# Kernel tuning notes

Hardware: AMD Instinct MI355X
Metric: run time of the kernel (lower is better)

The kernel has to match this reference:

```python
import jax, jax.numpy as jnp
import numpy as np

DT = 0.1
BOX = 1.0  # WORLD_SIZE
EPS = 1e-6


def range_angle(ang):
    return jnp.mod(ang + jnp.pi, 2.0 * jnp.pi) - jnp.pi


def ekf_step(x, P, a, Y, n1, n2_sigma, n2_kappa, gains, obs_gains):
    # x: (N,5) [px,py,ang,vel,ang_vel]; P: (N,5,5); a: (N,2); Y: (2,N)
    N = x.shape[0]
    dt = DT
    og = obs_gains

    # --- noise-free dynamics (w=0 in original forward) ---
    vel = gains[0] * a[:, 0]
    ang_vel = gains[1] * a[:, 1]
    ang = range_angle(x[:, 2] + ang_vel * dt)
    px = jnp.clip(x[:, 0] + vel * jnp.cos(ang) * dt, -BOX, BOX)
    py = jnp.clip(x[:, 1] + vel * jnp.sin(ang) * dt, -BOX, BOX)
    x_ = jnp.stack([px, py, ang, vel, ang_vel], axis=1)  # (N,5)

    # --- Jacobian A (N,5,5): eye(3) block + two trig entries ---
    d3 = jnp.arange(3)
    A = jnp.zeros((N, 5, 5), x.dtype)
    A = A.at[:, d3, d3].set(1.0)
    A = A.at[:, 0, 2].set(-vel * jnp.sin(ang) * dt)
    A = A.at[:, 1, 2].set(vel * jnp.cos(ang) * dt)

    # --- predict: L is identity in the original code, so L Q L^T = Q ---
    Q = jnp.diag(jnp.exp(2.0 * n1))
    P_ = jnp.einsum('nij,njk,nlk->nil', A, P, A) + Q  # (N,5,5)

    # --- innovation covariance S = H P_ H^T + M R M^T (R = I, M diag) ---
    # H = [0 | diag(og)] so H P_ H^T = diag(og) P_[3:5,3:5] diag(og)
    HPHt = P_[:, 3:5, 3:5] * og[None, :, None] * og[None, None, :]
    m_diag = x_[:, 3:5] ** 2 * jnp.exp(2.0 * n2_kappa) + jnp.exp(2.0 * n2_sigma)
    S = HPHt + m_diag[:, :, None] * jnp.eye(2, dtype=x.dtype)  # (N,2,2)

    # --- explicit 2x2 inverse ---
    sa, sb = S[:, 0, 0], S[:, 0, 1]
    sc, sd = S[:, 1, 0], S[:, 1, 1]
    det = sa * sd - sb * sc
    Sinv = jnp.stack([jnp.stack([sd, -sb], -1), jnp.stack([-sc, sa], -1)], -2)
    Sinv = Sinv / det[:, None, None]

    # --- Kalman gain K = P_ H^T S^{-1} ---
    PHt = P_[:, :, 3:5] * og[None, None, :]  # (N,5,2)
    K = jnp.einsum('nij,njk->nik', PHt, Sinv)  # (N,5,2)

    # --- update ---
    h = og[None, :] * x_[:, 3:5]  # noise-free observations (N,2)
    err = Y.T - h
    x_new = x_ + jnp.einsum('nij,nj->ni', K, err)

    KH = jnp.zeros((N, 5, 5), x.dtype).at[:, :, 3:5].set(K * og[None, None, :])
    I_KH = jnp.eye(5, dtype=x.dtype) - KH
    P_new = jnp.einsum('nij,njk->nik', I_KH, P_)
    P_new = 0.5 * (P_new + jnp.swapaxes(P_new, -1, -2)) + EPS * jnp.eye(5, dtype=x.dtype)
    return x_new, P_new, K


def setup_inputs() -> dict:
    key = jax.random.key(0)
    ks = jax.random.split(key, 6)
    N = 500_000
    x = jax.random.normal(ks[0], (N, 5), jnp.float32)
    # symmetric positive-definite covariances
    Lr = 0.1 * jax.random.normal(ks[1], (N, 5, 5), jnp.float32)
    P = jnp.einsum('nij,nkj->nik', Lr, Lr) + 0.5 * jnp.eye(5, dtype=jnp.float32)
    a = jax.random.normal(ks[2], (N, 2), jnp.float32)
    Y = 0.5 * jax.random.normal(ks[3], (2, N), jnp.float32)
    n1 = jnp.full((5,), -1.0, jnp.float32)
    n2 = jnp.full((4,), -1.0, jnp.float32)
    return {
        'x': x, 'P': P, 'a': a, 'Y': Y,
        'n1': n1,
        'n2_sigma': n2[:2],
        'n2_kappa': n2[2:],
        'gains': jnp.ones((2,), jnp.float32),
        'obs_gains': jnp.ones((2,), jnp.float32),
    }


def reference(x, P, a, Y, n1, n2_sigma, n2_kappa, gains, obs_gains):
    return ekf_step(x, P, a, Y, n1, n2_sigma, n2_kappa, gains, obs_gains)
```

## Files before the change

kernel.cpp:

```cpp
#include <hip/hip_runtime.h>
#include <math.h>
#include <stdint.h>


#define BLK 64
#define SLICE_F 2560

struct Pref {
    float4 p0, p1, p2, p3, p4, p5;
    float  pr;
    float4 x4;
    float  xr;
    float2 av;
    float  y0, y1;
};

__device__ __forceinline__ void load_pref(Pref& r,
    const float* __restrict__ Pg, const float* __restrict__ xg,
    const float* __restrict__ ag, const float* __restrict__ Yg,
    int N, int base, int l) {
    const float4* p4 = (const float4*)(Pg + (size_t)base * 25);
    r.p0 = p4[0 * 64 + l]; r.p1 = p4[1 * 64 + l]; r.p2 = p4[2 * 64 + l];
    r.p3 = p4[3 * 64 + l]; r.p4 = p4[4 * 64 + l]; r.p5 = p4[5 * 64 + l];
    r.pr = (Pg + (size_t)base * 25)[1536 + l];
    r.x4 = ((const float4*)(xg + (size_t)base * 5))[l];
    r.xr = (xg + (size_t)base * 5)[256 + l];
    r.av = ((const float2*)(ag + (size_t)base * 2))[l];
    r.y0 = Yg[base + l];
    r.y1 = Yg[N + base + l];
}

__device__ __forceinline__ void stage_write(const Pref& r, float* s, int l) {
    float4* s4 = (float4*)s;
    s4[0 * 64 + l] = r.p0; s4[1 * 64 + l] = r.p1; s4[2 * 64 + l] = r.p2;
    s4[3 * 64 + l] = r.p3; s4[4 * 64 + l] = r.p4; s4[5 * 64 + l] = r.p5;
    s[1536 + l] = r.pr;
    ((float4*)(s + 1600))[l] = r.x4;
    s[1856 + l] = r.xr;
}

struct EkfOut {
    float px, py, ang, xn3, xn4;
    float t00, s01, s02, t11, s12, t22, Pn33, Pn44;
    float K30, K41;
};

__device__ __forceinline__ EkfOut ekf_math(
    float x0, float x1, float x2, float a0, float a1, float y0, float y1,
    float p00, float p01, float p02, float p10, float p11, float p12,
    float p20, float p21, float p22,
    float g0, float g1, float og0, float og1,
    float q0, float q1, float q2, float q3, float q4,
    float e2s0, float e2s1, float e2k0, float e2k1)
{
    const float dt = 0.1f;
    const float fPI  = 3.14159265358979323846f;
    const float f2PI = 6.28318530717958647692f;
    const float EPS_ = 1e-6f;

    float vel = g0 * a0, angvel = g1 * a1;

    float ar = x2 + angvel * dt + fPI;
    float w = fmodf(ar, f2PI);
    if (w < 0.0f) w += f2PI;
    float ang = w - fPI;

    float s, c;
    sincosf(ang, &s, &c);

    EkfOut o;
    o.px = fminf(fmaxf(x0 + vel * c * dt, -1.0f), 1.0f);
    o.py = fminf(fmaxf(x1 + vel * s * dt, -1.0f), 1.0f);
    o.ang = ang;

    float m0 = -vel * s * dt, m1 = vel * c * dt;

    float b00 = p00 + m0 * p20, b01 = p01 + m0 * p21, b02 = p02 + m0 * p22;
    float b10 = p10 + m1 * p20, b11 = p11 + m1 * p21, b12 = p12 + m1 * p22;
    float t00 = b00 + m0 * b02, t01 = b01 + m1 * b02;
    float t10 = b10 + m0 * b12, t11 = b11 + m1 * b12;
    float t20 = p20 + m0 * p22, t21 = p21 + m1 * p22, t22 = p22;
    float t02 = b02, t12 = b12;

    t00 += q0; t11 += q1; t22 += q2;
    o.s01 = 0.5f * (t01 + t10);
    o.s02 = 0.5f * (t02 + t20);
    o.s12 = 0.5f * (t12 + t21);
    o.t00 = t00 + EPS_; o.t11 = t11 + EPS_; o.t22 = t22 + EPS_;

    float S00 = q3 * og0 * og0 + vel * vel * e2k0 + e2s0;
    float S11 = q4 * og1 * og1 + angvel * angvel * e2k1 + e2s1;
    o.K30 = q3 * og0 / S00;
    o.K41 = q4 * og1 / S11;

    o.xn3 = vel    + o.K30 * (y0 - og0 * vel);
    o.xn4 = angvel + o.K41 * (y1 - og1 * angvel);
    o.Pn33 = (1.0f - o.K30 * og0) * q3 + EPS_;
    o.Pn44 = (1.0f - o.K41 * og1) * q4 + EPS_;
    return o;
}

__global__ __launch_bounds__(256) void ekf_kernel(
    const float* __restrict__ xg, const float* __restrict__ Pg,
    const float* __restrict__ ag, const float* __restrict__ Yg,
    const float* __restrict__ n1, const float* __restrict__ n2s,
    const float* __restrict__ n2k, const float* __restrict__ gains,
    const float* __restrict__ og, float* __restrict__ out, int N)
{
    __shared__ float4 ldsv[4 * (SLICE_F / 4)];
    const int tid = threadIdx.x;
    const int wv = tid >> 6, l = tid & 63;
    float* s = (float*)ldsv + wv * SLICE_F;

    const int tiles = (N + BLK - 1) / BLK;
    const int NW = gridDim.x * 4;
    const int wp = blockIdx.x * 4 + wv;
    const int myTiles = (wp < tiles) ? (tiles - wp + NW - 1) / NW : 0;
    if (myTiles <= 0) return;

    const float g0 = gains[0], g1 = gains[1];
    const float og0 = og[0], og1 = og[1];
    const float q0 = expf(2.f * n1[0]), q1 = expf(2.f * n1[1]),
                q2 = expf(2.f * n1[2]), q3 = expf(2.f * n1[3]),
                q4 = expf(2.f * n1[4]);
    const float e2s0 = expf(2.f * n2s[0]), e2s1 = expf(2.f * n2s[1]);
    const float e2k0 = expf(2.f * n2k[0]), e2k1 = expf(2.f * n2k[1]);

    Pref A, B;
    {
        int b0 = wp * BLK;
        if (b0 + BLK <= N) load_pref(A, Pg, xg, ag, Yg, N, b0, l);
    }

    int k = 0;
    auto process = [&](Pref& cur, Pref& nxt) {
        const int base = (wp + k * NW) * BLK;
        if (base + BLK <= N) {
            stage_write(cur, s, l);
            if (k + 1 < myTiles) {
                int nb = (wp + (k + 1) * NW) * BLK;
                if (nb + BLK <= N) load_pref(nxt, Pg, xg, ag, Yg, N, nb, l);
            }
            const float* pr = s + l * 25;
            float p00 = pr[0], p01 = pr[1], p02 = pr[2];
            float p10 = pr[5], p11 = pr[6], p12 = pr[7];
            float p20 = pr[10], p21 = pr[11], p22 = pr[12];
            const float* xr = s + 1600 + l * 5;
            float x0 = xr[0], x1 = xr[1], x2 = xr[2];

            EkfOut o = ekf_math(x0, x1, x2, cur.av.x, cur.av.y, cur.y0, cur.y1,
                                p00, p01, p02, p10, p11, p12, p20, p21, p22,
                                g0, g1, og0, og1, q0, q1, q2, q3, q4,
                                e2s0, e2s1, e2k0, e2k1);

            float* xx = s + l * 5;
            xx[0] = o.px; xx[1] = o.py; xx[2] = o.ang; xx[3] = o.xn3; xx[4] = o.xn4;
            float* pp = s + 320 + l * 25;
            pp[0]  = o.t00; pp[1]  = o.s01; pp[2]  = o.s02; pp[3]  = 0.f; pp[4]  = 0.f;
            pp[5]  = o.s01; pp[6]  = o.t11; pp[7]  = o.s12; pp[8]  = 0.f; pp[9]  = 0.f;
            pp[10] = o.s02; pp[11] = o.s12; pp[12] = o.t22; pp[13] = 0.f; pp[14] = 0.f;
            pp[15] = 0.f;   pp[16] = 0.f;   pp[17] = 0.f;   pp[18] = o.Pn33; pp[19] = 0.f;
            pp[20] = 0.f;   pp[21] = 0.f;   pp[22] = 0.f;   pp[23] = 0.f;   pp[24] = o.Pn44;
            float* kk = s + 1920 + l * 10;
            kk[0] = 0.f; kk[1] = 0.f; kk[2] = 0.f; kk[3] = 0.f; kk[4] = 0.f;
            kk[5] = 0.f; kk[6] = o.K30; kk[7] = 0.f; kk[8] = 0.f; kk[9] = o.K41;

            float4* gx4 = (float4*)(out + (size_t)base * 5);
            float4* gp4 = (float4*)(out + (size_t)5 * N + (size_t)base * 25);
            float4* gk4 = (float4*)(out + (size_t)30 * N + (size_t)base * 10);
            const float4* lx4 = (const float4*)s;
            const float4* lp4 = (const float4*)(s + 320);
            const float4* lk4 = (const float4*)(s + 1920);
            gx4[l] = lx4[l];
            if (l < 16) gx4[64 + l] = lx4[64 + l];
            #pragma unroll
            for (int j = 0; j < 6; ++j) gp4[j * 64 + l] = lp4[j * 64 + l];
            if (l < 16) gp4[384 + l] = lp4[384 + l];
            #pragma unroll
            for (int j = 0; j < 2; ++j) gk4[j * 64 + l] = lk4[j * 64 + l];
            if (l < 32) gk4[128 + l] = lk4[128 + l];
        } else {
            const int i = base + l;
            if (i < N) {
                const float* pr = Pg + (size_t)i * 25;
                EkfOut o = ekf_math(xg[i * 5 + 0], xg[i * 5 + 1], xg[i * 5 + 2],
                                    ag[i * 2 + 0], ag[i * 2 + 1],
                                    Yg[i], Yg[N + i],
                                    pr[0], pr[1], pr[2], pr[5], pr[6], pr[7],
                                    pr[10], pr[11], pr[12],
                                    g0, g1, og0, og1, q0, q1, q2, q3, q4,
                                    e2s0, e2s1, e2k0, e2k1);
                float* gx = out + (size_t)i * 5;
                gx[0] = o.px; gx[1] = o.py; gx[2] = o.ang; gx[3] = o.xn3; gx[4] = o.xn4;
                float* gp = out + (size_t)5 * N + (size_t)i * 25;
                gp[0] = o.t00; gp[1] = o.s01; gp[2] = o.s02; gp[3] = 0.f; gp[4] = 0.f;
                gp[5] = o.s01; gp[6] = o.t11; gp[7] = o.s12; gp[8] = 0.f; gp[9] = 0.f;
                gp[10] = o.s02; gp[11] = o.s12; gp[12] = o.t22; gp[13] = 0.f; gp[14] = 0.f;
                gp[15] = 0.f; gp[16] = 0.f; gp[17] = 0.f; gp[18] = o.Pn33; gp[19] = 0.f;
                gp[20] = 0.f; gp[21] = 0.f; gp[22] = 0.f; gp[23] = 0.f; gp[24] = o.Pn44;
                float* gk = out + (size_t)30 * N + (size_t)i * 10;
                gk[0] = 0.f; gk[1] = 0.f; gk[2] = 0.f; gk[3] = 0.f; gk[4] = 0.f;
                gk[5] = 0.f; gk[6] = o.K30; gk[7] = 0.f; gk[8] = 0.f; gk[9] = o.K41;
            }
        }
    };

    while (true) {
        process(A, B);
        if (++k >= myTiles) break;
        process(B, A);
        if (++k >= myTiles) break;
    }
}

extern "C" void kernel_launch(void* const* d_in, const int* in_sizes, int n_in,
                              void* d_out, int out_size, void* d_ws, size_t ws_size,
                              hipStream_t stream) {
    const float* x     = (const float*)d_in[0];
    const float* P     = (const float*)d_in[1];
    const float* a     = (const float*)d_in[2];
    const float* Y     = (const float*)d_in[3];
    const float* n1    = (const float*)d_in[4];
    const float* n2s   = (const float*)d_in[5];
    const float* n2k   = (const float*)d_in[6];
    const float* gains = (const float*)d_in[7];
    const float* og    = (const float*)d_in[8];
    const int N = in_sizes[0] / 5;
    const int tiles = (N + BLK - 1) / BLK;
    int G = 768;
    if (G * 4 > tiles) G = (tiles + 3) / 4;
    ekf_kernel<<<G, 256, 0, stream>>>(x, P, a, Y, n1, n2s, n2k, gains, og,
                                      (float*)d_out, N);
}
```

Measured before the change: 171.8 us.

## Replace persistent grid-stride loop with one tile per wave, drop register prefetch

Each wavefront now handles exactly one 64-element tile and the grid is sized to cover all tiles, replacing the persistent 768-block grid-stride loop with software double-buffered register prefetch. The kernel should be simpler and less register-hungry, and occupancy and the hardware scheduler are relied on to hide memory latency instead of explicit prefetch. The trade is many more blocks to launch and re-evaluating the scalar parameter exps per wave.

```diff
diff --git a/kernel.cpp b/kernel.cpp
--- a/kernel.cpp
+++ b/kernel.cpp
@@ -5,100 +5,6 @@
 
 #define BLK 64
 #define SLICE_F 2560
-
-struct Pref {
-    float4 p0, p1, p2, p3, p4, p5;
-    float  pr;
-    float4 x4;
-    float  xr;
-    float2 av;
-    float  y0, y1;
-};
-
-__device__ __forceinline__ void load_pref(Pref& r,
-    const float* __restrict__ Pg, const float* __restrict__ xg,
-    const float* __restrict__ ag, const float* __restrict__ Yg,
-    int N, int base, int l) {
-    const float4* p4 = (const float4*)(Pg + (size_t)base * 25);
-    r.p0 = p4[0 * 64 + l]; r.p1 = p4[1 * 64 + l]; r.p2 = p4[2 * 64 + l];
-    r.p3 = p4[3 * 64 + l]; r.p4 = p4[4 * 64 + l]; r.p5 = p4[5 * 64 + l];
-    r.pr = (Pg + (size_t)base * 25)[1536 + l];
-    r.x4 = ((const float4*)(xg + (size_t)base * 5))[l];
-    r.xr = (xg + (size_t)base * 5)[256 + l];
-    r.av = ((const float2*)(ag + (size_t)base * 2))[l];
-    r.y0 = Yg[base + l];
-    r.y1 = Yg[N + base + l];
-}
-
-__device__ __forceinline__ void stage_write(const Pref& r, float* s, int l) {
-    float4* s4 = (float4*)s;
-    s4[0 * 64 + l] = r.p0; s4[1 * 64 + l] = r.p1; s4[2 * 64 + l] = r.p2;
-    s4[3 * 64 + l] = r.p3; s4[4 * 64 + l] = r.p4; s4[5 * 64 + l] = r.p5;
-    s[1536 + l] = r.pr;
-    ((float4*)(s + 1600))[l] = r.x4;
-    s[1856 + l] = r.xr;
-}
-
-struct EkfOut {
-    float px, py, ang, xn3, xn4;
-    float t00, s01, s02, t11, s12, t22, Pn33, Pn44;
-    float K30, K41;
-};
-
-__device__ __forceinline__ EkfOut ekf_math(
-    float x0, float x1, float x2, float a0, float a1, float y0, float y1,
-    float p00, float p01, float p02, float p10, float p11, float p12,
-    float p20, float p21, float p22,
-    float g0, float g1, float og0, float og1,
-    float q0, float q1, float q2, float q3, float q4,
-    float e2s0, float e2s1, float e2k0, float e2k1)
-{
-    const float dt = 0.1f;
-    const float fPI  = 3.14159265358979323846f;
-    const float f2PI = 6.28318530717958647692f;
-    const float EPS_ = 1e-6f;
-
-    float vel = g0 * a0, angvel = g1 * a1;
-
-    float ar = x2 + angvel * dt + fPI;
-    float w = fmodf(ar, f2PI);
-    if (w < 0.0f) w += f2PI;
-    float ang = w - fPI;
-
-    float s, c;
-    sincosf(ang, &s, &c);
-
-    EkfOut o;
-    o.px = fminf(fmaxf(x0 + vel * c * dt, -1.0f), 1.0f);
-    o.py = fminf(fmaxf(x1 + vel * s * dt, -1.0f), 1.0f);
-    o.ang = ang;
-
-    float m0 = -vel * s * dt, m1 = vel * c * dt;
-
-    float b00 = p00 + m0 * p20, b01 = p01 + m0 * p21, b02 = p02 + m0 * p22;
-    float b10 = p10 + m1 * p20, b11 = p11 + m1 * p21, b12 = p12 + m1 * p22;
-    float t00 = b00 + m0 * b02, t01 = b01 + m1 * b02;
-    float t10 = b10 + m0 * b12, t11 = b11 + m1 * b12;
-    float t20 = p20 + m0 * p22, t21 = p21 + m1 * p22, t22 = p22;
-    float t02 = b02, t12 = b12;
-
-    t00 += q0; t11 += q1; t22 += q2;
-    o.s01 = 0.5f * (t01 + t10);
-    o.s02 = 0.5f * (t02 + t20);
-    o.s12 = 0.5f * (t12 + t21);
-    o.t00 = t00 + EPS_; o.t11 = t11 + EPS_; o.t22 = t22 + EPS_;
-
-    float S00 = q3 * og0 * og0 + vel * vel * e2k0 + e2s0;
-    float S11 = q4 * og1 * og1 + angvel * angvel * e2k1 + e2s1;
-    o.K30 = q3 * og0 / S00;
-    o.K41 = q4 * og1 / S11;
-
-    o.xn3 = vel    + o.K30 * (y0 - og0 * vel);
-    o.xn4 = angvel + o.K41 * (y1 - og1 * angvel);
-    o.Pn33 = (1.0f - o.K30 * og0) * q3 + EPS_;
-    o.Pn44 = (1.0f - o.K41 * og1) * q4 + EPS_;
-    return o;
-}
 
 __global__ __launch_bounds__(256) void ekf_kernel(
     const float* __restrict__ xg, const float* __restrict__ Pg,
@@ -113,10 +19,14 @@
     float* s = (float*)ldsv + wv * SLICE_F;
 
     const int tiles = (N + BLK - 1) / BLK;
-    const int NW = gridDim.x * 4;
-    const int wp = blockIdx.x * 4 + wv;
-    const int myTiles = (wp < tiles) ? (tiles - wp + NW - 1) / NW : 0;
-    if (myTiles <= 0) return;
+    const int tile = blockIdx.x * 4 + wv;
+    if (tile >= tiles) return;
+    const int base = tile * BLK;
+
+    const float dt = 0.1f;
+    const float fPI  = 3.14159265358979323846f;
+    const float f2PI = 6.28318530717958647692f;
+    const float EPS_ = 1e-6f;
 
     const float g0 = gains[0], g1 = gains[1];
     const float og0 = og[0], og1 = og[1];
@@ -126,90 +36,152 @@
     const float e2s0 = expf(2.f * n2s[0]), e2s1 = expf(2.f * n2s[1]);
     const float e2k0 = expf(2.f * n2k[0]), e2k1 = expf(2.f * n2k[1]);
 
-    Pref A, B;
-    {
-        int b0 = wp * BLK;
-        if (b0 + BLK <= N) load_pref(A, Pg, xg, ag, Yg, N, b0, l);
-    }
-
-    int k = 0;
-    auto process = [&](Pref& cur, Pref& nxt) {
-        const int base = (wp + k * NW) * BLK;
-        if (base + BLK <= N) {
-            stage_write(cur, s, l);
-            if (k + 1 < myTiles) {
-                int nb = (wp + (k + 1) * NW) * BLK;
-                if (nb + BLK <= N) load_pref(nxt, Pg, xg, ag, Yg, N, nb, l);
-            }
-            const float* pr = s + l * 25;
-            float p00 = pr[0], p01 = pr[1], p02 = pr[2];
-            float p10 = pr[5], p11 = pr[6], p12 = pr[7];
+    if (base + BLK <= N) {
+        const float4* p4 = (const float4*)(Pg + (size_t)base * 25);
+        float4 v0 = p4[0 * 64 + l];
+        float4 v1 = p4[1 * 64 + l];
+        float4 v2 = p4[2 * 64 + l];
+        float4 v3 = p4[3 * 64 + l];
+        float4 v4 = p4[4 * 64 + l];
+        float4 v5 = p4[5 * 64 + l];
+        float  vr = (Pg + (size_t)base * 25)[1536 + l];
+        float4 xv = ((const float4*)(xg + (size_t)base * 5))[l];
+        float  xr = (xg + (size_t)base * 5)[256 + l];
+        float2 av = ((const float2*)(ag + (size_t)base * 2))[l];
+        float  y0 = Yg[base + l];
+        float  y1 = Yg[N + base + l];
+
+        float4* s4 = (float4*)s;
+        s4[0 * 64 + l] = v0; s4[1 * 64 + l] = v1; s4[2 * 64 + l] = v2;
+        s4[3 * 64 + l] = v3; s4[4 * 64 + l] = v4; s4[5 * 64 + l] = v5;
+        s[1536 + l] = vr;
+        ((float4*)(s + 1600))[l] = xv;
+        s[1856 + l] = xr;
+
+        const float* pr = s + l * 25;
+        float p00 = pr[0],  p01 = pr[1],  p02 = pr[2];
+        float p10 = pr[5],  p11 = pr[6],  p12 = pr[7];
+        float p20 = pr[10], p21 = pr[11], p22 = pr[12];
+        const float* xp = s + 1600 + l * 5;
+        float x0 = xp[0], x1 = xp[1], x2 = xp[2];
+
+        float vel = g0 * av.x, angvel = g1 * av.y;
+
+        float ar = x2 + angvel * dt + fPI;
+        float w = fmodf(ar, f2PI);
+        if (w < 0.0f) w += f2PI;
+        float ang = w - fPI;
+
+        float sn, cs;
+        sincosf(ang, &sn, &cs);
+
+        float px = fminf(fmaxf(x0 + vel * cs * dt, -1.0f), 1.0f);
+        float py = fminf(fmaxf(x1 + vel * sn * dt, -1.0f), 1.0f);
+
+        float m0 = -vel * sn * dt, m1 = vel * cs * dt;
+
+        float b00 = p00 + m0 * p20, b01 = p01 + m0 * p21, b02 = p02 + m0 * p22;
+        float b10 = p10 + m1 * p20, b11 = p11 + m1 * p21, b12 = p12 + m1 * p22;
+        float t00 = b00 + m0 * b02, t01 = b01 + m1 * b02;
+        float t10 = b10 + m0 * b12, t11 = b11 + m1 * b12;
+        float t20 = p20 + m0 * p22, t21 = p21 + m1 * p22, t22 = p22;
+        float t02 = b02, t12 = b12;
+
+        t00 += q0; t11 += q1; t22 += q2;
+        float s01 = 0.5f * (t01 + t10);
+        float s02 = 0.5f * (t02 + t20);
+        float s12 = 0.5f * (t12 + t21);
+        t00 += EPS_; t11 += EPS_; t22 += EPS_;
+
+        float S00 = q3 * og0 * og0 + vel * vel * e2k0 + e2s0;
+        float S11 = q4 * og1 * og1 + angvel * angvel * e2k1 + e2s1;
+        float K30 = q3 * og0 / S00;
+        float K41 = q4 * og1 / S11;
+
+        float xn3 = vel    + K30 * (y0 - og0 * vel);
+        float xn4 = angvel + K41 * (y1 - og1 * angvel);
+        float Pn33 = (1.0f - K30 * og0) * q3 + EPS_;
+        float Pn44 = (1.0f - K41 * og1) * q4 + EPS_;
+
+        float* xx = s + l * 5;
+        xx[0] = px; xx[1] = py; xx[2] = ang; xx[3] = xn3; xx[4] = xn4;
+        float* pp = s + 320 + l * 25;
+        pp[0]  = t00; pp[1]  = s01; pp[2]  = s02; pp[3]  = 0.f; pp[4]  = 0.f;
+        pp[5]  = s01; pp[6]  = t11; pp[7]  = s12; pp[8]  = 0.f; pp[9]  = 0.f;
+        pp[10] = s02; pp[11] = s12; pp[12] = t22; pp[13] = 0.f; pp[14] = 0.f;
+        pp[15] = 0.f; pp[16] = 0.f; pp[17] = 0.f; pp[18] = Pn33; pp[19] = 0.f;
+        pp[20] = 0.f; pp[21] = 0.f; pp[22] = 0.f; pp[23] = 0.f; pp[24] = Pn44;
+        float* kk = s + 1920 + l * 10;
+        kk[0] = 0.f; kk[1] = 0.f; kk[2] = 0.f; kk[3] = 0.f; kk[4] = 0.f;
+        kk[5] = 0.f; kk[6] = K30; kk[7] = 0.f; kk[8] = 0.f; kk[9] = K41;
+
+        float4* gx4 = (float4*)(out + (size_t)base * 5);
+        float4* gp4 = (float4*)(out + (size_t)5 * N + (size_t)base * 25);
+        float4* gk4 = (float4*)(out + (size_t)30 * N + (size_t)base * 10);
+        const float4* lx4 = (const float4*)s;
+        const float4* lp4 = (const float4*)(s + 320);
+        const float4* lk4 = (const float4*)(s + 1920);
+        gx4[l] = lx4[l];
+        if (l < 16) gx4[64 + l] = lx4[64 + l];
+        #pragma unroll
+        for (int j = 0; j < 6; ++j) gp4[j * 64 + l] = lp4[j * 64 + l];
+        if (l < 16) gp4[384 + l] = lp4[384 + l];
+        #pragma unroll
+        for (int j = 0; j < 2; ++j) gk4[j * 64 + l] = lk4[j * 64 + l];
+        if (l < 32) gk4[128 + l] = lk4[128 + l];
+    } else {
+        const int i = base + l;
+        if (i < N) {
+            const float* pr = Pg + (size_t)i * 25;
+            float p00 = pr[0],  p01 = pr[1],  p02 = pr[2];
+            float p10 = pr[5],  p11 = pr[6],  p12 = pr[7];
             float p20 = pr[10], p21 = pr[11], p22 = pr[12];
-            const float* xr = s + 1600 + l * 5;
-            float x0 = xr[0], x1 = xr[1], x2 = xr[2];
-
-            EkfOut o = ekf_math(x0, x1, x2, cur.av.x, cur.av.y, cur.y0, cur.y1,
-                                p00, p01, p02, p10, p11, p12, p20, p21, p22,
-                                g0, g1, og0, og1, q0, q1, q2, q3, q4,
-                                e2s0, e2s1, e2k0, e2k1);
-
-            float* xx = s + l * 5;
-            xx[0] = o.px; xx[1] = o.py; xx[2] = o.ang; xx[3] = o.xn3; xx[4] = o.xn4;
-            float* pp = s + 320 + l * 25;
-            pp[0]  = o.t00; pp[1]  = o.s01; pp[2]  = o.s02; pp[3]  = 0.f; pp[4]  = 0.f;
-            pp[5]  = o.s01; pp[6]  = o.t11; pp[7]  = o.s12; pp[8]  = 0.f; pp[9]  = 0.f;
-            pp[10] = o.s02; pp[11] = o.s12; pp[12] = o.t22; pp[13] = 0.f; pp[14] = 0.f;
-            pp[15] = 0.f;   pp[16] = 0.f;   pp[17] = 0.f;   pp[18] = o.Pn33; pp[19] = 0.f;
-            pp[20] = 0.f;   pp[21] = 0.f;   pp[22] = 0.f;   pp[23] = 0.f;   pp[24] = o.Pn44;
-            float* kk = s + 1920 + l * 10;
-            kk[0] = 0.f; kk[1] = 0.f; kk[2] = 0.f; kk[3] = 0.f; kk[4] = 0.f;
-            kk[5] = 0.f; kk[6] = o.K30; kk[7] = 0.f; kk[8] = 0.f; kk[9] = o.K41;
-
-            float4* gx4 = (float4*)(out + (size_t)base * 5);
-            float4* gp4 = (float4*)(out + (size_t)5 * N + (size_t)base * 25);
-            float4* gk4 = (float4*)(out + (size_t)30 * N + (size_t)base * 10);
-            const float4* lx4 = (const float4*)s;
-            const float4* lp4 = (const float4*)(s + 320);
-            const float4* lk4 = (const float4*)(s + 1920);
-            gx4[l] = lx4[l];
-            if (l < 16) gx4[64 + l] = lx4[64 + l];
-            #pragma unroll
-            for (int j = 0; j < 6; ++j) gp4[j * 64 + l] = lp4[j * 64 + l];
-            if (l < 16) gp4[384 + l] = lp4[384 + l];
-            #pragma unroll
-            for (int j = 0; j < 2; ++j) gk4[j * 64 + l] = lk4[j * 64 + l];
-            if (l < 32) gk4[128 + l] = lk4[128 + l];
-        } else {
-            const int i = base + l;
-            if (i < N) {
-                const float* pr = Pg + (size_t)i * 25;
-                EkfOut o = ekf_math(xg[i * 5 + 0], xg[i * 5 + 1], xg[i * 5 + 2],
-                                    ag[i * 2 + 0], ag[i * 2 + 1],
-                                    Yg[i], Yg[N + i],
-                                    pr[0], pr[1], pr[2], pr[5], pr[6], pr[7],
-                                    pr[10], pr[11], pr[12],
-                                    g0, g1, og0, og1, q0, q1, q2, q3, q4,
-                                    e2s0, e2s1, e2k0, e2k1);
-                float* gx = out + (size_t)i * 5;
-                gx[0] = o.px; gx[1] = o.py; gx[2] = o.ang; gx[3] = o.xn3; gx[4] = o.xn4;
-                float* gp = out + (size_t)5 * N + (size_t)i * 25;
-                gp[0] = o.t00; gp[1] = o.s01; gp[2] = o.s02; gp[3] = 0.f; gp[4] = 0.f;
-                gp[5] = o.s01; gp[6] = o.t11; gp[7] = o.s12; gp[8] = 0.f; gp[9] = 0.f;
-                gp[10] = o.s02; gp[11] = o.s12; gp[12] = o.t22; gp[13] = 0.f; gp[14] = 0.f;
-                gp[15] = 0.f; gp[16] = 0.f; gp[17] = 0.f; gp[18] = o.Pn33; gp[19] = 0.f;
-                gp[20] = 0.f; gp[21] = 0.f; gp[22] = 0.f; gp[23] = 0.f; gp[24] = o.Pn44;
-                float* gk = out + (size_t)30 * N + (size_t)i * 10;
-                gk[0] = 0.f; gk[1] = 0.f; gk[2] = 0.f; gk[3] = 0.f; gk[4] = 0.f;
-                gk[5] = 0.f; gk[6] = o.K30; gk[7] = 0.f; gk[8] = 0.f; gk[9] = o.K41;
-            }
+            float x0 = xg[i * 5 + 0], x1 = xg[i * 5 + 1], x2 = xg[i * 5 + 2];
+            float a0 = ag[i * 2 + 0], a1 = ag[i * 2 + 1];
+            float y0 = Yg[i], y1 = Yg[N + i];
+
+            float vel = g0 * a0, angvel = g1 * a1;
+            float ar = x2 + angvel * dt + fPI;
+            float w = fmodf(ar, f2PI);
+            if (w < 0.0f) w += f2PI;
+            float ang = w - fPI;
+            float sn, cs;
+            sincosf(ang, &sn, &cs);
+            float px = fminf(fmaxf(x0 + vel * cs * dt, -1.0f), 1.0f);
+            float py = fminf(fmaxf(x1 + vel * sn * dt, -1.0f), 1.0f);
+            float m0 = -vel * sn * dt, m1 = vel * cs * dt;
+            float b00 = p00 + m0 * p20, b01 = p01 + m0 * p21, b02 = p02 + m0 * p22;
+            float b10 = p10 + m1 * p20, b11 = p11 + m1 * p21, b12 = p12 + m1 * p22;
+            float t00 = b00 + m0 * b02, t01 = b01 + m1 * b02;
+            float t10 = b10 + m0 * b12, t11 = b11 + m1 * b12;
+            float t20 = p20 + m0 * p22, t21 = p21 + m1 * p22, t22 = p22;
+            float t02 = b02, t12 = b12;
+            t00 += q0; t11 += q1; t22 += q2;
+            float s01 = 0.5f * (t01 + t10);
+            float s02 = 0.5f * (t02 + t20);
+            float s12 = 0.5f * (t12 + t21);
+            t00 += EPS_; t11 += EPS_; t22 += EPS_;
+            float S00 = q3 * og0 * og0 + vel * vel * e2k0 + e2s0;
+            float S11 = q4 * og1 * og1 + angvel * angvel * e2k1 + e2s1;
+            float K30 = q3 * og0 / S00;
+            float K41 = q4 * og1 / S11;
+            float xn3 = vel    + K30 * (y0 - og0 * vel);
+            float xn4 = angvel + K41 * (y1 - og1 * angvel);
+            float Pn33 = (1.0f - K30 * og0) * q3 + EPS_;
+            float Pn44 = (1.0f - K41 * og1) * q4 + EPS_;
+
+            float* gx = out + (size_t)i * 5;
+            gx[0] = px; gx[1] = py; gx[2] = ang; gx[3] = xn3; gx[4] = xn4;
+            float* gp = out + (size_t)5 * N + (size_t)i * 25;
+            gp[0] = t00; gp[1] = s01; gp[2] = s02; gp[3] = 0.f; gp[4] = 0.f;
+            gp[5] = s01; gp[6] = t11; gp[7] = s12; gp[8] = 0.f; gp[9] = 0.f;
+            gp[10] = s02; gp[11] = s12; gp[12] = t22; gp[13] = 0.f; gp[14] = 0.f;
+            gp[15] = 0.f; gp[16] = 0.f; gp[17] = 0.f; gp[18] = Pn33; gp[19] = 0.f;
+            gp[20] = 0.f; gp[21] = 0.f; gp[22] = 0.f; gp[23] = 0.f; gp[24] = Pn44;
+            float* gk = out + (size_t)30 * N + (size_t)i * 10;
+            gk[0] = 0.f; gk[1] = 0.f; gk[2] = 0.f; gk[3] = 0.f; gk[4] = 0.f;
+            gk[5] = 0.f; gk[6] = K30; gk[7] = 0.f; gk[8] = 0.f; gk[9] = K41;
         }
-    };
-
-    while (true) {
-        process(A, B);
-        if (++k >= myTiles) break;
-        process(B, A);
-        if (++k >= myTiles) break;
     }
 }
 
@@ -227,8 +199,7 @@
     const float* og    = (const float*)d_in[8];
     const int N = in_sizes[0] / 5;
     const int tiles = (N + BLK - 1) / BLK;
-    int G = 768;
-    if (G * 4 > tiles) G = (tiles + 3) / 4;
+    const int G = (tiles + 3) / 4;
     ekf_kernel<<<G, 256, 0, stream>>>(x, P, a, Y, n1, n2s, n2k, gains, og,
                                       (float*)d_out, N);
 }
```

Result: faster. 148.7 us (-13.4%).
